# Performance work log

Hardware: AMD Instinct MI355X
Metric: run time of the kernel (lower is better)

## Reference

```python
import jax, jax.numpy as jnp
import numpy as np


def setup_inputs() -> dict:
    key = jax.random.key(0)
    ks = jax.random.split(key, 12)
    B, IN, H = 4096, 512, 1024
    s = lambda k, shape, scale: jax.random.normal(k, shape, dtype=jnp.float32) * scale
    inp = {
        "inputs": s(ks[0], (B, IN), 1.0),
        "h0": s(ks[1], (B, H), 1.0),
        "c0": s(ks[2], (B, H), 1.0),
        "ts": jax.random.uniform(ks[3], (B, 2), dtype=jnp.float32),
        "w_ih": s(ks[4], (4 * H, IN), 1.0 / np.sqrt(IN)),
        "w_hh": s(ks[5], (4 * H, H), 1.0 / np.sqrt(H)),
        "b_ih": s(ks[6], (4 * H,), 1.0 / np.sqrt(H)),
        "b_hh": s(ks[7], (4 * H,), 1.0 / np.sqrt(H)),
        "w1": s(ks[8], (H, H), 1.0 / np.sqrt(H)),
        "b1": s(ks[9], (H,), 1.0 / np.sqrt(H)),
        "w2": s(ks[10], (H, H), 1.0 / np.sqrt(H)),
        "b2": s(ks[11], (H,), 1.0 / np.sqrt(H)),
    }
    return inp


def _lstm_cell(x, h, c, w_ih, w_hh, b_ih, b_hh):
    # gates: [B, 4H] in PyTorch (i, f, g, o) order
    gates = x @ w_ih.T + h @ w_hh.T + b_ih + b_hh
    i, f, g, o = jnp.split(gates, 4, axis=-1)
    i, f, o = jax.nn.sigmoid(i), jax.nn.sigmoid(f), jax.nn.sigmoid(o)
    g = jnp.tanh(g)
    c_new = f * c + i * g
    h_new = o * jnp.tanh(c_new)
    return h_new, c_new


def reference(inputs, h0, c0, ts, w_ih, w_hh, b_ih, b_hh, w1, b1, w2, b2):
    # Two stacked LSTMCell applications sharing the same weights
    h, c = _lstm_cell(inputs, h0, c0, w_ih, w_hh, b_ih, b_hh)
    h, c = _lstm_cell(inputs, h, c, w_ih, w_hh, b_ih, b_hh)

    # Autonomous ODE func: Linear -> Tanh -> Linear
    f = lambda y: jnp.tanh(y @ w1.T + b1) @ w2.T + b2

    # One RK4 step per sample from ts[:,0] to ts[:,1] (batched, no python loop)
    dt = (ts[:, 1] - ts[:, 0])[:, None]  # [B, 1]
    k1 = f(h)
    k2 = f(h + 0.5 * dt * k1)
    k3 = f(h + 0.5 * dt * k2)
    k4 = f(h + dt * k3)
    ht = h + (dt / 6.0) * (k1 + 2.0 * k2 + 2.0 * k3 + k4)
    return (ht, c)
```

## Files before the change

### kernel.cpp

```cpp
#include <hip/hip_runtime.h>

typedef short short8 __attribute__((ext_vector_type(8)));
typedef float f32x4 __attribute__((ext_vector_type(4)));
typedef unsigned short u16x8 __attribute__((ext_vector_type(8)));

#define B_DIM 4096
#define IN_DIM 512
#define H_DIM 1024
#define KCAT 1536

__device__ __forceinline__ float bs2f(unsigned short s) {
    return __uint_as_float(((unsigned int)s) << 16);
}
__device__ __forceinline__ unsigned short f2bs(float f) {
    unsigned int u = __float_as_uint(f);
    u += 0x7fff + ((u >> 16) & 1);
    return (unsigned short)(u >> 16);
}
__device__ __forceinline__ float sigm(float x) { return 1.0f / (1.0f + __expf(-x)); }
__device__ __forceinline__ float ftanh(float x) { return 1.0f - 2.0f / (__expf(2.0f * x) + 1.0f); }

__device__ __forceinline__ int gperm(int r) {
    int g = r >> 10, j = r & 1023;
    return ((j >> 4) << 6) + (g << 4) + (j & 15);
}

#define T0 262144
#define T1 786432
#define T2 1048576
#define T3 1572864
#define T4 1703936
#define T5 1835008
__device__ __forceinline__ u16x8 cvt8(const float* __restrict__ in, long i) {
    float4 a = *(const float4*)(in + i);
    float4 b = *(const float4*)(in + i + 4);
    u16x8 o;
    o[0] = f2bs(a.x); o[1] = f2bs(a.y); o[2] = f2bs(a.z); o[3] = f2bs(a.w);
    o[4] = f2bs(b.x); o[5] = f2bs(b.y); o[6] = f2bs(b.z); o[7] = f2bs(b.w);
    return o;
}
__global__ __launch_bounds__(256) void pack_all(const float* __restrict__ x,
                                                const float* __restrict__ h0,
                                                const float* __restrict__ wih,
                                                const float* __restrict__ whh,
                                                const float* __restrict__ w1,
                                                const float* __restrict__ w2,
                                                unsigned short* __restrict__ xb,
                                                unsigned short* __restrict__ hb0,
                                                unsigned short* __restrict__ wcat,
                                                unsigned short* __restrict__ w116,
                                                unsigned short* __restrict__ w216) {
    long g = (long)blockIdx.x * 256 + threadIdx.x;
    if (g < T0) {
        long i = g * 8;
        *(u16x8*)(xb + i) = cvt8(x, i);
    } else if (g < T1) {
        long i = (g - T0) * 8;
        *(u16x8*)(hb0 + i) = cvt8(h0, i);
    } else if (g < T2) {
        long i = (g - T1) * 8;
        int r = (int)(i / IN_DIM), c = (int)(i % IN_DIM);
        *(u16x8*)(wcat + (size_t)gperm(r) * KCAT + c) = cvt8(wih, i);
    } else if (g < T3) {
        long i = (g - T2) * 8;
        int r = (int)(i / H_DIM), c = (int)(i % H_DIM);
        *(u16x8*)(wcat + (size_t)gperm(r) * KCAT + IN_DIM + c) = cvt8(whh, i);
    } else if (g < T4) {
        long i = (g - T3) * 8;
        *(u16x8*)(w116 + i) = cvt8(w1, i);
    } else if (g < T5) {
        long i = (g - T4) * 8;
        *(u16x8*)(w216 + i) = cvt8(w2, i);
    }
}

__global__ __launch_bounds__(256) void transp_w2(const float* __restrict__ w2,
                                                 unsigned short* __restrict__ w2t) {
    int tid = blockIdx.x * 256 + threadIdx.x;
    int t = tid & 1023;
    int jb = tid >> 10;
    float4 a = *(const float4*)(w2 + (size_t)t * H_DIM + jb * 8);
    float4 b = *(const float4*)(w2 + (size_t)t * H_DIM + jb * 8 + 4);
    float v[8] = {a.x, a.y, a.z, a.w, b.x, b.y, b.z, b.w};
    #pragma unroll
    for (int q = 0; q < 8; ++q)
        w2t[(size_t)(jb * 8 + q) * H_DIM + t] = f2bs(v[q]);
}

__global__ __launch_bounds__(256) void bck(const float* __restrict__ b2,
                                           const float* __restrict__ w1,
                                           float* __restrict__ bc) {
    __shared__ float ws[4];
    int n = blockIdx.x;
    int t = threadIdx.x;
    float4 bv = *(const float4*)(b2 + t * 4);
    float4 wv = *(const float4*)(w1 + (size_t)n * H_DIM + t * 4);
    float p = bv.x * wv.x + bv.y * wv.y + bv.z * wv.z + bv.w * wv.w;
    #pragma unroll
    for (int off = 32; off > 0; off >>= 1) p += __shfl_down(p, off);
    if ((t & 63) == 0) ws[t >> 6] = p;
    __syncthreads();
    if (t == 0) bc[n] = ws[0] + ws[1] + ws[2] + ws[3];
}

__global__ __launch_bounds__(256) void prep_small(const float* __restrict__ bih,
                                                  const float* __restrict__ bhh,
                                                  const float* __restrict__ ts,
                                                  float* __restrict__ bsum,
                                                  float* __restrict__ dtv,
                                                  int n4h, int nb) {
    int i = blockIdx.x * blockDim.x + threadIdx.x;
    if (i < n4h) bsum[gperm(i)] = bih[i] + bhh[i];
    if (i < nb)  dtv[i] = ts[2 * i + 1] - ts[2 * i];
}

#define NT8 (KCAT / 32)

__global__ __launch_bounds__(512) void gemm8(
    const unsigned short* __restrict__ xb,
    const unsigned short* __restrict__ hb,
    const unsigned short* __restrict__ W,
    const float* __restrict__ bias,
    unsigned short* __restrict__ h_out,
    float* __restrict__ c_out,
    const float* __restrict__ c_in) {
    __shared__ unsigned short lA[3][128 * 32];
    __shared__ unsigned short lB[3][256 * 32];
    const int t = threadIdx.x;
    const int lane = t & 63;
    const int wave = t >> 6;
    const int wm = (wave >> 2) * 64;
    const int wn = (wave & 3) * 64;
    const int fr = lane & 15;
    const int kb = lane >> 4;
    const int tile_m = blockIdx.y * 128;
    const int tile_n = blockIdx.x * 256;

    f32x4 acc[4][4];
    #pragma unroll
    for (int i = 0; i < 4; ++i)
        #pragma unroll
        for (int j = 0; j < 4; ++j)
            acc[i][j] = (f32x4){0.f, 0.f, 0.f, 0.f};

    auto stageA = [&](int kt) {
        const int buf = kt % 3;
        int row = t >> 2;
        int g = t & 3;
        int gs = g ^ ((row >> 1) & 3);
        int kk = kt * 32 + gs * 8;
        const unsigned short* src = (kk < IN_DIM)
            ? xb + (size_t)(tile_m + row) * IN_DIM + kk
            : hb + (size_t)(tile_m + row) * H_DIM + (kk - IN_DIM);
        __builtin_amdgcn_global_load_lds(
            (__attribute__((address_space(1))) void*)src,
            (__attribute__((address_space(3))) void*)(&lA[buf][row * 32 + g * 8]), 16, 0, 0);
    };
    auto stageB = [&](int kt) {
        const int buf = kt % 3;
        #pragma unroll
        for (int j = 0; j < 2; ++j) {
            int idx = j * 512 + t;
            int row = idx >> 2;
            int g = idx & 3;
            int gs = g ^ ((row >> 1) & 3);
            int kk = kt * 32 + gs * 8;
            __builtin_amdgcn_global_load_lds(
                (__attribute__((address_space(1))) void*)(W + (size_t)(tile_n + row) * KCAT + kk),
                (__attribute__((address_space(3))) void*)(&lB[buf][row * 32 + g * 8]), 16, 0, 0);
        }
    };

    stageA(0); stageB(0);
    stageA(1); stageB(1);

    for (int kt = 0; kt < NT8; ++kt) {
        const int buf = kt % 3;
        if (kt + 1 < NT8) asm volatile("s_waitcnt vmcnt(3)" ::: "memory");
        else              asm volatile("s_waitcnt vmcnt(0)" ::: "memory");
        __builtin_amdgcn_s_barrier();
        asm volatile("" ::: "memory");
        short8 bfr[4], af[4];
        #pragma unroll
        for (int j = 0; j < 4; ++j) {
            int brow = wn + j * 16 + fr;
            bfr[j] = *(const short8*)&lB[buf][brow * 32 + (kb ^ ((brow >> 1) & 3)) * 8];
        }
        #pragma unroll
        for (int i = 0; i < 4; ++i) {
            int arow = wm + i * 16 + fr;
            af[i] = *(const short8*)&lA[buf][arow * 32 + (kb ^ ((arow >> 1) & 3)) * 8];
        }
        __builtin_amdgcn_s_setprio(1);
        #pragma unroll
        for (int i = 0; i < 4; ++i)
            #pragma unroll
            for (int j = 0; j < 4; ++j)
                acc[i][j] = __builtin_amdgcn_mfma_f32_16x16x32_bf16(af[i], bfr[j], acc[i][j], 0, 0, 0);
        __builtin_amdgcn_s_setprio(0);
        if (kt + 2 < NT8) { stageA(kt + 2); stageB(kt + 2); }
        asm volatile("" ::: "memory");
    }

    const int jbase = ((tile_n + wn) >> 6) << 4;
    float bv[4];
    #pragma unroll
    for (int g = 0; g < 4; ++g) bv[g] = bias[tile_n + wn + g * 16 + fr];
    #pragma unroll
    for (int i = 0; i < 4; ++i) {
        #pragma unroll
        for (int r = 0; r < 4; ++r) {
            const int m = tile_m + wm + i * 16 + kb * 4 + r;
            const int j = jbase + fr;
            float ig = sigm(acc[i][0][r] + bv[0]);
            float fg = sigm(acc[i][1][r] + bv[1]);
            float gg = ftanh(acc[i][2][r] + bv[2]);
            float og = sigm(acc[i][3][r] + bv[3]);
            float cin = c_in[(size_t)m * H_DIM + j];
            float cn = fg * cin + ig * gg;
            float hn = og * ftanh(cn);
            h_out[(size_t)m * H_DIM + j] = f2bs(hn);
            c_out[(size_t)m * H_DIM + j] = cn;
        }
    }
}

template <int EPI>
__global__ __launch_bounds__(256) void gemm2(
    const unsigned short* __restrict__ A1,
    const unsigned short* __restrict__ W,
    const int M, const int N, const int K,
    const float* __restrict__ bias,
    unsigned short* __restrict__ outb,
    float* __restrict__ outf,
    const float* __restrict__ z1f,
    float* __restrict__ Uf,
    const unsigned short* __restrict__ hmat,
    const float* __restrict__ dtv,
    const float alpha, const float cw, const int first, const int last) {
    constexpr int BM = 64, BN = 64, BK = 64;
    constexpr int MR = 2, NR = 2;
    __shared__ unsigned short lA[2][BM * BK];
    __shared__ unsigned short lB[2][BN * BK];
    const int t = threadIdx.x;
    const int lane = t & 63;
    const int wave = t >> 6;
    const int wm = (wave >> 1) * 32;
    const int wn = (wave & 1) * 32;
    const int fr = lane & 15;
    const int kb = lane >> 4;
    const int tile_m = blockIdx.y * BM;
    const int tile_n = blockIdx.x * BN;

    f32x4 acc[MR][NR];
    #pragma unroll
    for (int i = 0; i < MR; ++i)
        #pragma unroll
        for (int j = 0; j < NR; ++j)
            acc[i][j] = (f32x4){0.f, 0.f, 0.f, 0.f};

    const unsigned short* aptr1 = A1 + (size_t)tile_m * K;
    const unsigned short* wptr  = W + (size_t)tile_n * K;

    auto stage = [&](int kt) {
        const int buf = kt & 1;
        const int k0 = kt * BK;
        #pragma unroll
        for (int j = 0; j < 2; ++j) {
            int idx = j * 256 + t;
            int row = idx >> 3;
            int g = idx & 7;
            int col = (g ^ (row & 7)) * 8;
            __builtin_amdgcn_global_load_lds(
                (__attribute__((address_space(1))) void*)(aptr1 + (size_t)row * K + k0 + col),
                (__attribute__((address_space(3))) void*)(&lA[buf][row * BK + g * 8]), 16, 0, 0);
        }
        #pragma unroll
        for (int j = 0; j < 2; ++j) {
            int idx = j * 256 + t;
            int row = idx >> 3;
            int g = idx & 7;
            int col = (g ^ (row & 7)) * 8;
            __builtin_amdgcn_global_load_lds(
                (__attribute__((address_space(1))) void*)(wptr + (size_t)row * K + k0 + col),
                (__attribute__((address_space(3))) void*)(&lB[buf][row * BK + g * 8]), 16, 0, 0);
        }
    };

    const int NT = K / BK;
    stage(0);
    for (int kt = 0; kt < NT; ++kt) {
        const int buf = kt & 1;
        asm volatile("s_waitcnt vmcnt(0)" ::: "memory");
        __builtin_amdgcn_s_barrier();
        asm volatile("" ::: "memory");
        short8 af[2][MR], bfr[2][NR];
        #pragma unroll
        for (int h = 0; h < 2; ++h) {
            #pragma unroll
            for (int i = 0; i < MR; ++i) {
                int arow = wm + i * 16 + fr;
                int gidx = h * 4 + kb;
                af[h][i] = *(const short8*)&lA[buf][arow * BK + (gidx ^ (arow & 7)) * 8];
            }
            #pragma unroll
            for (int j = 0; j < NR; ++j) {
                int brow = wn + j * 16 + fr;
                int gidx = h * 4 + kb;
                bfr[h][j] = *(const short8*)&lB[buf][brow * BK + (gidx ^ (brow & 7)) * 8];
            }
        }
        if (kt + 1 < NT) stage(kt + 1);
        #pragma unroll
        for (int h = 0; h < 2; ++h)
            #pragma unroll
            for (int i = 0; i < MR; ++i)
                #pragma unroll
                for (int j = 0; j < NR; ++j)
                    acc[i][j] = __builtin_amdgcn_mfma_f32_16x16x32_bf16(af[h][i], bfr[h][j], acc[i][j], 0, 0, 0);
        asm volatile("" ::: "memory");
    }

    #pragma unroll
    for (int i = 0; i < MR; ++i) {
        #pragma unroll
        for (int r = 0; r < 4; ++r) {
            const int m = tile_m + wm + i * 16 + kb * 4 + r;
            float dt = 0.f;
            if (EPI >= 6) dt = dtv[m];
            #pragma unroll
            for (int j = 0; j < NR; ++j) {
                const int n = tile_n + wn + j * 16 + fr;
                const size_t off = (size_t)m * N + n;
                float v = acc[i][j][r];
                if (EPI == 0) {
                    if (bias) v += bias[n];
                    outb[off] = f2bs(v);
                } else if (EPI == 5) {
                    v += bias[n];
                    outf[off] = v;
                    outb[off] = f2bs(ftanh(v));
                } else if (EPI == 6) {
                    v += bias[n];
                    float z1v = z1f[off];
                    float z = z1v + alpha * dt * v;
                    float u = ftanh(z);
                    if (first) {
                        Uf[off] = ftanh(z1v) + cw * u;
                        outb[off] = f2bs(u);
                    } else if (last) {
                        outb[off] = f2bs(Uf[off] + cw * u);
                    } else {
                        Uf[off] = Uf[off] + cw * u;
                        outb[off] = f2bs(u);
                    }
                } else {
                    float hv = bs2f(hmat[off]);
                    outf[off] = hv + dt * (v * (1.0f / 6.0f) + bias[n]);
                }
            }
        }
    }
}

extern "C" void kernel_launch(void* const* d_in, const int* in_sizes, int n_in,
                              void* d_out, int out_size, void* d_ws, size_t ws_size,
                              hipStream_t stream) {
    int IX = 0, IH0 = 1, IC0 = 2, ITS = 3, IWIH = 4, IWHH = 5, IBIH = 6, IBHH = 7,
        IW1 = 8, IB1 = 9, IW2 = 10, IB2 = 11;
    const bool sorted_ok = n_in >= 12 &&
        in_sizes[0] == 1024 && in_sizes[1] == 1024 && in_sizes[2] == 4096 &&
        in_sizes[3] == 4096 && in_sizes[4] == 4194304 && in_sizes[5] == 4194304 &&
        in_sizes[6] == 2097152 && in_sizes[7] == 8192 && in_sizes[8] == 1048576 &&
        in_sizes[9] == 1048576 && in_sizes[10] == 4194304 && in_sizes[11] == 2097152;
    if (sorted_ok) {
        IB1 = 0; IB2 = 1; IBHH = 2; IBIH = 3; IC0 = 4; IH0 = 5;
        IX = 6; ITS = 7; IW1 = 8; IW2 = 9; IWHH = 10; IWIH = 11;
    }
    const float* x_f   = (const float*)d_in[IX];
    const float* h0_f  = (const float*)d_in[IH0];
    const float* c0_f  = (const float*)d_in[IC0];
    const float* ts_f  = (const float*)d_in[ITS];
    const float* wih_f = (const float*)d_in[IWIH];
    const float* whh_f = (const float*)d_in[IWHH];
    const float* bih_f = (const float*)d_in[IBIH];
    const float* bhh_f = (const float*)d_in[IBHH];
    const float* w1_f  = (const float*)d_in[IW1];
    const float* b1_f  = (const float*)d_in[IB1];
    const float* w2_f  = (const float*)d_in[IW2];
    const float* b2_f  = (const float*)d_in[IB2];

    constexpr size_t SZ_BIN  = (size_t)B_DIM * IN_DIM;
    constexpr size_t SZ_BH   = (size_t)B_DIM * H_DIM;
    constexpr size_t SZ_HH   = (size_t)H_DIM * H_DIM;
    constexpr size_t SZ_WCAT = (size_t)4 * H_DIM * KCAT;

    float* bsum = (float*)d_ws;
    float* dtv  = bsum + 4 * H_DIM;
    float* bc   = dtv + B_DIM;
    float* S    = bc + H_DIM;
    float* c1f  = S + SZ_BH;
    unsigned short* wcat = (unsigned short*)(c1f + SZ_BH);
    unsigned short* w116 = wcat + SZ_WCAT;
    unsigned short* w216 = w116 + SZ_HH;
    unsigned short* w2t  = w216 + SZ_HH;
    unsigned short* wc16 = w2t + SZ_HH;
    unsigned short* xb   = wc16 + SZ_HH;
    unsigned short* hb0  = xb + SZ_BIN;
    unsigned short* hb1  = hb0 + SZ_BH;
    unsigned short* hb2  = hb1 + SZ_BH;
    unsigned short* ubuf = hb2 + SZ_BH;
    unsigned short* ybuf = ubuf + SZ_BH;

    float* out_ht = (float*)d_out;
    float* out_c  = out_ht + SZ_BH;
    float* z1f = S;
    float* Uf  = c1f;

    const int TB = 256;
    pack_all<<<T5 / TB, TB, 0, stream>>>(x_f, h0_f, wih_f, whh_f, w1_f, w2_f,
                                         xb, hb0, wcat, w116, w216);
    transp_w2<<<(H_DIM * H_DIM / 8) / TB, TB, 0, stream>>>(w2_f, w2t);
    prep_small<<<(4 * H_DIM) / TB, TB, 0, stream>>>(bih_f, bhh_f, ts_f, bsum, dtv, 4 * H_DIM, B_DIM);
    bck<<<H_DIM, TB, 0, stream>>>(b2_f, w1_f, bc);

    dim3 g8(4 * H_DIM / 256, B_DIM / 128);
    dim3 gSm(H_DIM / 64, B_DIM / 64);
    dim3 gWc(H_DIM / 64, H_DIM / 64);

    gemm2<0><<<gWc, TB, 0, stream>>>(w116, w2t, H_DIM, H_DIM, H_DIM, nullptr,
                                     wc16, nullptr, nullptr, nullptr, nullptr, nullptr, 0.f, 0.f, 0, 0);

    gemm8<<<g8, 512, 0, stream>>>(xb, hb0, wcat, bsum, hb1, S, c0_f);
    gemm8<<<g8, 512, 0, stream>>>(xb, hb1, wcat, bsum, hb2, out_c, S);

    gemm2<5><<<gSm, TB, 0, stream>>>(hb2, w116, B_DIM, H_DIM, H_DIM, b1_f,
                                     ubuf, z1f, nullptr, nullptr, nullptr, nullptr, 0.f, 0.f, 0, 0);
    gemm2<6><<<gSm, TB, 0, stream>>>(ubuf, wc16, B_DIM, H_DIM, H_DIM, bc,
                                     ybuf, nullptr, z1f, Uf, nullptr, dtv, 0.5f, 2.0f, 1, 0);
    gemm2<6><<<gSm, TB, 0, stream>>>(ybuf, wc16, B_DIM, H_DIM, H_DIM, bc,
                                     ubuf, nullptr, z1f, Uf, nullptr, dtv, 0.5f, 2.0f, 0, 0);
    gemm2<6><<<gSm, TB, 0, stream>>>(ubuf, wc16, B_DIM, H_DIM, H_DIM, bc,
                                     hb1, nullptr, z1f, Uf, nullptr, dtv, 1.0f, 1.0f, 0, 1);
    gemm2<7><<<gSm, TB, 0, stream>>>(hb1, w216, B_DIM, H_DIM, H_DIM, b2_f,
                                     nullptr, out_ht, nullptr, nullptr, hb2, dtv, 0.f, 0.f, 0, 0);
}
```

Measured before the change: 281.2 us.

## Precompute shared input projection once and reuse it across both LSTM steps

Splits the fused LSTM GEMM: one kernel computes x@W_ih plus bias into a bf16 gate buffer, and both recurrent steps run a GEMM with K equal to H only. Each step adds the stored input gates in its epilogue. This removes the repeated x@W_ih work in the second LSTM step. In exchange it writes and then twice re-reads a large B×4H intermediate, which costs extra memory traffic and adds bf16 rounding of the pre-activation input term.

```diff
diff --git a/kernel.cpp b/kernel.cpp
--- a/kernel.cpp
+++ b/kernel.cpp
@@ -114,16 +114,17 @@
     if (i < nb)  dtv[i] = ts[2 * i + 1] - ts[2 * i];
 }
 
-#define NT8 (KCAT / 32)
-
+template <int MODE>
 __global__ __launch_bounds__(512) void gemm8(
-    const unsigned short* __restrict__ xb,
-    const unsigned short* __restrict__ hb,
+    const unsigned short* __restrict__ A,
     const unsigned short* __restrict__ W,
     const float* __restrict__ bias,
+    unsigned short* __restrict__ gx,
     unsigned short* __restrict__ h_out,
     float* __restrict__ c_out,
     const float* __restrict__ c_in) {
+    constexpr int KA = (MODE == 0) ? IN_DIM : H_DIM;
+    constexpr int NT = KA / 32;
     __shared__ unsigned short lA[3][128 * 32];
     __shared__ unsigned short lB[3][256 * 32];
     const int t = threadIdx.x;
@@ -149,11 +150,8 @@
         int g = t & 3;
         int gs = g ^ ((row >> 1) & 3);
         int kk = kt * 32 + gs * 8;
-        const unsigned short* src = (kk < IN_DIM)
-            ? xb + (size_t)(tile_m + row) * IN_DIM + kk
-            : hb + (size_t)(tile_m + row) * H_DIM + (kk - IN_DIM);
         __builtin_amdgcn_global_load_lds(
-            (__attribute__((address_space(1))) void*)src,
+            (__attribute__((address_space(1))) void*)(A + (size_t)(tile_m + row) * KA + kk),
             (__attribute__((address_space(3))) void*)(&lA[buf][row * 32 + g * 8]), 16, 0, 0);
     };
     auto stageB = [&](int kt) {
@@ -174,10 +172,10 @@
     stageA(0); stageB(0);
     stageA(1); stageB(1);
 
-    for (int kt = 0; kt < NT8; ++kt) {
+    for (int kt = 0; kt < NT; ++kt) {
         const int buf = kt % 3;
-        if (kt + 1 < NT8) asm volatile("s_waitcnt vmcnt(3)" ::: "memory");
-        else              asm volatile("s_waitcnt vmcnt(0)" ::: "memory");
+        if (kt + 1 < NT) asm volatile("s_waitcnt vmcnt(3)" ::: "memory");
+        else             asm volatile("s_waitcnt vmcnt(0)" ::: "memory");
         __builtin_amdgcn_s_barrier();
         asm volatile("" ::: "memory");
         short8 bfr[4], af[4];
@@ -198,29 +196,46 @@
             for (int j = 0; j < 4; ++j)
                 acc[i][j] = __builtin_amdgcn_mfma_f32_16x16x32_bf16(af[i], bfr[j], acc[i][j], 0, 0, 0);
         __builtin_amdgcn_s_setprio(0);
-        if (kt + 2 < NT8) { stageA(kt + 2); stageB(kt + 2); }
+        if (kt + 2 < NT) { stageA(kt + 2); stageB(kt + 2); }
         asm volatile("" ::: "memory");
     }
 
     const int jbase = ((tile_n + wn) >> 6) << 4;
-    float bv[4];
-    #pragma unroll
-    for (int g = 0; g < 4; ++g) bv[g] = bias[tile_n + wn + g * 16 + fr];
-    #pragma unroll
-    for (int i = 0; i < 4; ++i) {
-        #pragma unroll
-        for (int r = 0; r < 4; ++r) {
-            const int m = tile_m + wm + i * 16 + kb * 4 + r;
-            const int j = jbase + fr;
-            float ig = sigm(acc[i][0][r] + bv[0]);
-            float fg = sigm(acc[i][1][r] + bv[1]);
-            float gg = ftanh(acc[i][2][r] + bv[2]);
-            float og = sigm(acc[i][3][r] + bv[3]);
-            float cin = c_in[(size_t)m * H_DIM + j];
-            float cn = fg * cin + ig * gg;
-            float hn = og * ftanh(cn);
-            h_out[(size_t)m * H_DIM + j] = f2bs(hn);
-            c_out[(size_t)m * H_DIM + j] = cn;
+    if (MODE == 0) {
+        float bv[4];
+        #pragma unroll
+        for (int g = 0; g < 4; ++g) bv[g] = bias[tile_n + wn + g * 16 + fr];
+        #pragma unroll
+        for (int i = 0; i < 4; ++i) {
+            #pragma unroll
+            for (int r = 0; r < 4; ++r) {
+                const int m = tile_m + wm + i * 16 + kb * 4 + r;
+                #pragma unroll
+                for (int g = 0; g < 4; ++g)
+                    gx[(size_t)m * 4096 + tile_n + wn + g * 16 + fr] = f2bs(acc[i][g][r] + bv[g]);
+            }
+        }
+    } else {
+        #pragma unroll
+        for (int i = 0; i < 4; ++i) {
+            #pragma unroll
+            for (int r = 0; r < 4; ++r) {
+                const int m = tile_m + wm + i * 16 + kb * 4 + r;
+                const int j = jbase + fr;
+                float vg[4];
+                #pragma unroll
+                for (int g = 0; g < 4; ++g)
+                    vg[g] = acc[i][g][r] + bs2f(gx[(size_t)m * 4096 + tile_n + wn + g * 16 + fr]);
+                float ig = sigm(vg[0]);
+                float fg = sigm(vg[1]);
+                float gg = ftanh(vg[2]);
+                float og = sigm(vg[3]);
+                float cin = c_in[(size_t)m * H_DIM + j];
+                float cn = fg * cin + ig * gg;
+                float hn = og * ftanh(cn);
+                h_out[(size_t)m * H_DIM + j] = f2bs(hn);
+                c_out[(size_t)m * H_DIM + j] = cn;
+            }
         }
     }
 }
@@ -392,6 +407,7 @@
 
     constexpr size_t SZ_BIN  = (size_t)B_DIM * IN_DIM;
     constexpr size_t SZ_BH   = (size_t)B_DIM * H_DIM;
+    constexpr size_t SZ_B4H  = (size_t)B_DIM * 4 * H_DIM;
     constexpr size_t SZ_HH   = (size_t)H_DIM * H_DIM;
     constexpr size_t SZ_WCAT = (size_t)4 * H_DIM * KCAT;
 
@@ -411,6 +427,7 @@
     unsigned short* hb2  = hb1 + SZ_BH;
     unsigned short* ubuf = hb2 + SZ_BH;
     unsigned short* ybuf = ubuf + SZ_BH;
+    unsigned short* Gx   = ybuf + SZ_BH;
 
     float* out_ht = (float*)d_out;
     float* out_c  = out_ht + SZ_BH;
@@ -431,8 +448,10 @@
     gemm2<0><<<gWc, TB, 0, stream>>>(w116, w2t, H_DIM, H_DIM, H_DIM, nullptr,
                                      wc16, nullptr, nullptr, nullptr, nullptr, nullptr, 0.f, 0.f, 0, 0);
 
-    gemm8<<<g8, 512, 0, stream>>>(xb, hb0, wcat, bsum, hb1, S, c0_f);
-    gemm8<<<g8, 512, 0, stream>>>(xb, hb1, wcat, bsum, hb2, out_c, S);
+    gemm8<0><<<g8, 512, 0, stream>>>(xb, wcat, bsum, Gx, nullptr, nullptr, nullptr);
+
+    gemm8<1><<<g8, 512, 0, stream>>>(hb0, wcat + IN_DIM, nullptr, Gx, hb1, S, c0_f);
+    gemm8<1><<<g8, 512, 0, stream>>>(hb1, wcat + IN_DIM, nullptr, Gx, hb2, out_c, S);
 
     gemm2<5><<<gSm, TB, 0, stream>>>(hb2, w116, B_DIM, H_DIM, H_DIM, b1_f,
                                      ubuf, z1f, nullptr, nullptr, nullptr, nullptr, 0.f, 0.f, 0, 0);
```

Result: no change. 277.9 us (-1.2%).
